# Performance work log

Measured on AMD Instinct MI355X. Metric: run time of the kernel, lower is better.

## Reference

```python
import jax, jax.numpy as jnp
import numpy as np

C = 768
H = 12
HD = C // H  # 64


def setup_inputs() -> dict:
    key = jax.random.key(0)
    k1, k2, k3, k4, k5, k6 = jax.random.split(key, 6)
    B, T = 8, 1024
    x = jax.random.normal(k1, (B, T, C), dtype=jnp.float32)
    mask = jax.random.randint(k2, (B, T), 0, 2, dtype=jnp.int32)
    # Linear params stored so that y = x @ W + b (W is [in, out])
    W_attn = jax.random.normal(k3, (C, 3 * C), dtype=jnp.float32) * 0.02
    b_attn = jax.random.normal(k4, (3 * C,), dtype=jnp.float32) * 0.02
    W_proj = jax.random.normal(k5, (C, C), dtype=jnp.float32) * 0.02
    b_proj = jax.random.normal(k6, (C,), dtype=jnp.float32) * 0.02
    return {"x": x, "mask": mask, "W_attn": W_attn, "b_attn": b_attn,
            "W_proj": W_proj, "b_proj": b_proj}


def reference(x, mask, W_attn, b_attn, W_proj, b_proj):
    B, T, _ = x.shape
    qkv = x @ W_attn + b_attn                      # [B, T, 3C]
    q, k, v = jnp.split(qkv, 3, axis=2)            # each [B, T, C]
    # [B, T, C] -> [B, H, T, HD]
    q = q.reshape(B, T, H, HD).transpose(0, 2, 1, 3)
    k = k.reshape(B, T, H, HD).transpose(0, 2, 1, 3)
    v = v.reshape(B, T, H, HD).transpose(0, 2, 1, 3)

    scale = 1.0 / np.sqrt(HD).astype(np.float32)
    att = jnp.einsum('bhqd,bhkd->bhqk', q, k) * scale  # [B, H, T, T]

    causal = jnp.tril(jnp.ones((T, T), dtype=bool))    # [T, T]
    att = jnp.where(causal[None, None], att, -jnp.inf)

    # custom mask: per-(batch, query-row) flag; where mask==0 the whole row
    # of scores is overwritten with 0.0001 (AFTER causal fill, as in torch)
    row_masked = (mask == 0)[:, None, :, None]         # [B, 1, T, 1]
    att = jnp.where(row_masked, jnp.float32(1e-4), att)

    att = jax.nn.softmax(att, axis=-1)
    # dropout layers are identity in eval mode
    y = jnp.einsum('bhqk,bhkd->bhqd', att, v)          # [B, H, T, HD]
    y = y.transpose(0, 2, 1, 3).reshape(B, T, C)
    y = y @ W_proj + b_proj
    return y
```

## Files before the change

kernel.cpp:

```cpp
#include <hip/hip_runtime.h>
#include <hip/hip_bf16.h>

#define BQ 8
#define TT 1024
#define CC 768
#define NH 12
#define HD 64
#define BH (BQ*NH)
#define MROWS (BQ*TT)
#define NQKV (3*CC)
#define KD CC

typedef unsigned short u16;
typedef __attribute__((ext_vector_type(4))) short short4v;
typedef __attribute__((ext_vector_type(8))) short short8v;
typedef __attribute__((ext_vector_type(4))) float floatx4;
typedef __attribute__((address_space(1))) const unsigned int gu32;
typedef __attribute__((address_space(3))) unsigned int lu32;

__device__ __forceinline__ float bf2f(u16 u) {
  union { unsigned int i; float f; } c; c.i = ((unsigned int)u) << 16; return c.f;
}
__device__ __forceinline__ u16 f2bf(float f) {
  union { __hip_bfloat16 h; u16 u; } c;
  c.h = __float2bfloat16(f);
  return c.u;
}
__device__ __forceinline__ float fast_exp2(float x) {
  return __builtin_amdgcn_exp2f(x);
}
__device__ __forceinline__ void async_ld16(const u16* g, u16* l) {
  __builtin_amdgcn_global_load_lds((gu32*)g, (lu32*)l, 16, 0, 0);
}

#define PREP_CONV 6144
#define PREP_WA   1728
#define PREP_WP   576
#define PREP_TOTAL (PREP_CONV + PREP_WA + PREP_WP)

__global__ __launch_bounds__(256) void prep_kernel(
    const float* __restrict__ x, u16* __restrict__ xb,
    const float* __restrict__ Wattn, u16* __restrict__ WtA,
    const float* __restrict__ Wproj, u16* __restrict__ WtP,
    float* __restrict__ mvz)
{
  __shared__ float tile[32][33];
  int bid = blockIdx.x;
  int tid = threadIdx.x;
  if (bid == PREP_TOTAL) {
    for (int i = tid; i < BH * HD; i += 256) mvz[i] = 0.f;
    return;
  }
  if (bid < PREP_CONV) {
    int i = (bid * 256 + tid) * 4;
    floatx4 v = *(const floatx4*)(x + i);
    short4v o;
    o[0] = (short)f2bf(v[0]); o[1] = (short)f2bf(v[1]);
    o[2] = (short)f2bf(v[2]); o[3] = (short)f2bf(v[3]);
    *(short4v*)(xb + i) = o;
    return;
  }
  const float* in; u16* out; int R, Cc, b2;
  if (bid < PREP_CONV + PREP_WA) { in = Wattn; out = WtA; R = KD; Cc = NQKV; b2 = bid - PREP_CONV; }
  else                           { in = Wproj; out = WtP; R = CC; Cc = CC;   b2 = bid - PREP_CONV - PREP_WA; }
  int ct = Cc >> 5;
  int bx = b2 % ct;
  int by = b2 / ct;
  int tx = tid & 31;
  int ty = tid >> 5;
  int c0 = bx << 5, r0 = by << 5;
#pragma unroll
  for (int s = 0; s < 4; ++s)
    tile[ty + s*8][tx] = in[(size_t)(r0 + ty + s*8) * Cc + c0 + tx];
  __syncthreads();
#pragma unroll
  for (int s = 0; s < 4; ++s)
    out[(size_t)(c0 + ty + s*8) * R + r0 + tx] = f2bf(tile[tx][ty + s*8]);
}

__global__ __launch_bounds__(256) void gemm_bt(
    const u16* __restrict__ A, const u16* __restrict__ Bt,
    const float* __restrict__ bias,
    float* __restrict__ out,
    u16* __restrict__ qo, u16* __restrict__ ko, u16* __restrict__ vo,
    float* __restrict__ mvp,
    int M, int N, int mode)
{
  __shared__ u16 smem[64 * 64 + 128 * 64];
  u16* Asm = smem;
  u16* Bsm = smem + 64 * 64;

  int tid = threadIdx.x;
  int lane = tid & 63;
  int w = tid >> 6;
  int c = lane & 15;
  int q4 = lane >> 4;

  int mtiles = M >> 6;
  int mt = blockIdx.x % mtiles;
  int nt = blockIdx.x / mtiles;
  int m0 = mt << 6, n0 = nt << 7;

  int wr = (w >> 1) << 5;
  int wc = (w & 1) << 6;

  int srow8 = lane >> 3;
  int ug = ((lane & 7) ^ srow8) << 3;
  const u16* ag = A  + (size_t)(m0 + w * 16 + srow8) * KD + ug;
  const u16* bg = Bt + (size_t)(n0 + w * 32 + srow8) * KD + ug;
  u16* asl = &Asm[(w * 16) * 64];
  u16* bsl = &Bsm[(w * 32) * 64];

  floatx4 acc[2][4];
#pragma unroll
  for (int mi = 0; mi < 2; ++mi)
#pragma unroll
    for (int ni = 0; ni < 4; ++ni) acc[mi][ni] = (floatx4){0.f, 0.f, 0.f, 0.f};

  int c7 = c & 7;

#pragma unroll 1
  for (int kt = 0; kt < KD; kt += 64) {
    async_ld16(ag + kt,              asl);
    async_ld16(ag + kt + 8 * KD,     asl + 8 * 64);
    async_ld16(bg + kt,              bsl);
    async_ld16(bg + kt + 8 * KD,     bsl + 8 * 64);
    async_ld16(bg + kt + 16 * KD,    bsl + 16 * 64);
    async_ld16(bg + kt + 24 * KD,    bsl + 24 * 64);
    __syncthreads();

    short8v af[2][2], bf[4][2];
#pragma unroll
    for (int kc = 0; kc < 2; ++kc) {
      int uoff = ((kc * 4 + q4) ^ c7) << 3;
#pragma unroll
      for (int mi = 0; mi < 2; ++mi)
        af[mi][kc] = *(const short8v*)&Asm[(wr + mi * 16 + c) * 64 + uoff];
#pragma unroll
      for (int ni = 0; ni < 4; ++ni)
        bf[ni][kc] = *(const short8v*)&Bsm[(wc + ni * 16 + c) * 64 + uoff];
    }
#pragma unroll
    for (int kc = 0; kc < 2; ++kc)
#pragma unroll
      for (int mi = 0; mi < 2; ++mi)
#pragma unroll
        for (int ni = 0; ni < 4; ++ni)
          acc[mi][ni] = __builtin_amdgcn_mfma_f32_16x16x32_bf16(af[mi][kc], bf[ni][kc], acc[mi][ni], 0, 0, 0);
    __syncthreads();
  }

  if (mode == 0) {
    int which = (n0 + wc) / CC;
    int nbase = (n0 + wc) - which * CC;
    int bb = m0 >> 10;
    int t0 = m0 & 1023;

    if (which < 2) {
      u16* dst0 = (which == 0) ? qo : ko;
#pragma unroll
      for (int ni = 0; ni < 4; ++ni) {
        int nn = nbase + ni * 16 + c;
        int hh = nn >> 6, dd = nn & 63;
        float bv = bias[which * CC + nn];
#pragma unroll
        for (int mi = 0; mi < 2; ++mi) {
#pragma unroll
          for (int r = 0; r < 4; ++r) {
            int tt2 = t0 + wr + mi * 16 + q4 * 4 + r;
            dst0[(((size_t)(bb * NH + hh)) * TT + tt2) * HD + dd] = f2bf(acc[mi][ni][r] + bv);
          }
        }
      }
    }
    if (n0 + 127 >= 2 * CC) {
      u16* Ct = smem;
      if (which == 2) {
#pragma unroll
        for (int ni = 0; ni < 4; ++ni) {
          float bv = bias[2 * CC + nbase + ni * 16 + c];
#pragma unroll
          for (int mi = 0; mi < 2; ++mi) {
            short4v pk;
#pragma unroll
            for (int r = 0; r < 4; ++r) pk[r] = (short)f2bf(acc[mi][ni][r] + bv);
            *(short4v*)&Ct[(wc + ni * 16 + c) * 72 + wr + mi * 16 + q4 * 4] = pk;
          }
        }
      }
      __syncthreads();
#pragma unroll
      for (int j = 0; j < 4; ++j) {
        int flat = tid + j * 256;
        int drow = flat >> 3, u = flat & 7;
        int nn2 = n0 + drow;
        if (nn2 >= 2 * CC) {
          int nv = nn2 - 2 * CC;
          int h2 = nv >> 6, d2 = nv & 63;
          short8v val = *(const short8v*)&Ct[drow * 72 + u * 8];
          *(short8v*)&vo[(((size_t)(bb * NH + h2)) * HD + d2) * TT + t0 + u * 8] = val;
        }
      }
      if (which == 2) {
        int hw = nbase >> 6;
        int bhw = bb * NH + hw;
#pragma unroll
        for (int ni = 0; ni < 4; ++ni) {
          float bv = bias[2 * CC + nbase + ni * 16 + c];
          float s = 8.0f * bv;
#pragma unroll
          for (int mi = 0; mi < 2; ++mi)
#pragma unroll
            for (int r = 0; r < 4; ++r) s += acc[mi][ni][r];
          s += __shfl_xor(s, 16);
          s += __shfl_xor(s, 32);
          if (q4 == 0) atomicAdd(&mvp[bhw * HD + ni * 16 + c], s);
        }
      }
    }
  } else {
#pragma unroll
    for (int ni = 0; ni < 4; ++ni) {
      int nn = n0 + wc + ni * 16 + c;
      float bv = bias[nn];
#pragma unroll
      for (int mi = 0; mi < 2; ++mi) {
#pragma unroll
        for (int r = 0; r < 4; ++r) {
          int mm = m0 + wr + mi * 16 + q4 * 4 + r;
          out[(size_t)mm * N + nn] = acc[mi][ni][r] + bv;
        }
      }
    }
  }
}

__global__ __launch_bounds__(256) void gemm_proj(
    const u16* __restrict__ A, const u16* __restrict__ Bt,
    const float* __restrict__ bias, float* __restrict__ out)
{
  __shared__ u16 As[64 * 64];
  __shared__ u16 Bs[64 * 64];

  int tid = threadIdx.x;
  int lane = tid & 63;
  int w = tid >> 6;
  int c = lane & 15;
  int q4 = lane >> 4;

  int mt = blockIdx.x & 127;
  int nt = blockIdx.x >> 7;
  int m0 = mt << 6, n0 = nt << 6;

  int wr = (w >> 1) << 5;
  int wc = (w & 1) << 5;

  int srow8 = lane >> 3;
  int ug = ((lane & 7) ^ srow8) << 3;
  const u16* ag = A  + (size_t)(m0 + w * 16 + srow8) * KD + ug;
  const u16* bg = Bt + (size_t)(n0 + w * 16 + srow8) * KD + ug;
  u16* asl = &As[(w * 16) * 64];
  u16* bsl = &Bs[(w * 16) * 64];

  floatx4 acc[2][2];
#pragma unroll
  for (int mi = 0; mi < 2; ++mi)
#pragma unroll
    for (int ni = 0; ni < 2; ++ni) acc[mi][ni] = (floatx4){0.f, 0.f, 0.f, 0.f};

  int c7 = c & 7;

#pragma unroll 1
  for (int kt = 0; kt < KD; kt += 64) {
    async_ld16(ag + kt,          asl);
    async_ld16(ag + kt + 8 * KD, asl + 8 * 64);
    async_ld16(bg + kt,          bsl);
    async_ld16(bg + kt + 8 * KD, bsl + 8 * 64);
    __syncthreads();

    short8v af[2][2], bf[2][2];
#pragma unroll
    for (int kc = 0; kc < 2; ++kc) {
      int uoff = ((kc * 4 + q4) ^ c7) << 3;
#pragma unroll
      for (int mi = 0; mi < 2; ++mi)
        af[mi][kc] = *(const short8v*)&As[(wr + mi * 16 + c) * 64 + uoff];
#pragma unroll
      for (int ni = 0; ni < 2; ++ni)
        bf[ni][kc] = *(const short8v*)&Bs[(wc + ni * 16 + c) * 64 + uoff];
    }
#pragma unroll
    for (int kc = 0; kc < 2; ++kc)
#pragma unroll
      for (int mi = 0; mi < 2; ++mi)
#pragma unroll
        for (int ni = 0; ni < 2; ++ni)
          acc[mi][ni] = __builtin_amdgcn_mfma_f32_16x16x32_bf16(af[mi][kc], bf[ni][kc], acc[mi][ni], 0, 0, 0);
    __syncthreads();
  }

#pragma unroll
  for (int ni = 0; ni < 2; ++ni) {
    int nn = n0 + wc + ni * 16 + c;
    float bv = bias[nn];
#pragma unroll
    for (int mi = 0; mi < 2; ++mi) {
#pragma unroll
      for (int r = 0; r < 4; ++r) {
        int mm = m0 + wr + mi * 16 + q4 * 4 + r;
        out[(size_t)mm * CC + nn] = acc[mi][ni][r] + bv;
      }
    }
  }
}

#define LDW 72
#define SCL 0.18033688f

__global__ __launch_bounds__(256, 3) void attn_kernel(
    const u16* __restrict__ qb, const u16* __restrict__ kb,
    const u16* __restrict__ vtb, const int* __restrict__ mask,
    const float* __restrict__ meanv,
    u16* __restrict__ outb)
{
  __shared__ u16 Ks[2][64 * LDW];
  __shared__ u16 Vs[2][64 * LDW];
  __shared__ u16 Ps[4][16 * LDW];

  int tid = threadIdx.x;
  int lane = tid & 63;
  int w = tid >> 6;
  int c = lane & 15;
  int q4 = lane >> 4;

  int lbid = ((blockIdx.x & 7) * 96) + (blockIdx.x >> 3);
  int pair = lbid & 7;
  int bh = lbid >> 3;
  int b = bh / NH;
  int h = bh - b * NH;

  int qtA = pair;
  int qtB = 15 - pair;
  int rowbaseA = (qtA << 6) + (w << 4);
  int rowbaseB = (qtB << 6) + (w << 4);

  int srow = tid >> 2;
  int schunk = (tid & 3) << 4;
  const u16* kgp = kb + ((size_t)bh * TT + srow) * HD + schunk;
  const u16* vgp = vtb + ((size_t)bh * HD + srow) * TT + schunk;
  u16* pw = &Ps[w][0];

  short8v onesv;
#pragma unroll
  for (int j = 0; j < 8; ++j) onesv[j] = (short)0x3F80;

  short8v qfA[2], qfB[2];
  {
    const u16* qpA = qb + ((size_t)bh * TT + rowbaseA + c) * HD + q4 * 8;
    qfA[0] = *(const short8v*)qpA;
    qfA[1] = *(const short8v*)(qpA + 32);
    const u16* qpB = qb + ((size_t)bh * TT + rowbaseB + c) * HD + q4 * 8;
    qfB[0] = *(const short8v*)qpB;
    qfB[1] = *(const short8v*)(qpB + 32);
  }

  floatx4 oA[4], oB[4];
#pragma unroll
  for (int i = 0; i < 4; ++i) {
    oA[i] = (floatx4){0.f, 0.f, 0.f, 0.f};
    oB[i] = (floatx4){0.f, 0.f, 0.f, 0.f};
  }
  floatx4 o5A = (floatx4){0.f, 0.f, 0.f, 0.f};
  floatx4 o5B = (floatx4){0.f, 0.f, 0.f, 0.f};

  short8v kr0 = *(const short8v*)kgp;
  short8v kr1 = *(const short8v*)(kgp + 8);
  short8v vr0 = *(const short8v*)vgp;
  short8v vr1 = *(const short8v*)(vgp + 8);
  {
    u16* kd = &Ks[0][srow * LDW + schunk];
    u16* vd = &Vs[0][srow * LDW + schunk];
    *(short8v*)kd = kr0; *(short8v*)(kd + 8) = kr1;
    *(short8v*)vd = vr0; *(short8v*)(vd + 8) = vr1;
  }

  int qrl = (w << 4) + c;

#pragma unroll 1
  for (int kt = 0; kt <= qtB; ++kt) {
    int cur = kt & 1;
    __syncthreads();

    if (kt < qtB) {
      const u16* kp = kgp + ((size_t)(kt + 1) << 6) * HD;
      const u16* vp = vgp + ((kt + 1) << 6);
      kr0 = *(const short8v*)kp;
      kr1 = *(const short8v*)(kp + 8);
      vr0 = *(const short8v*)vp;
      vr1 = *(const short8v*)(vp + 8);
    }

    bool doA = (kt <= qtA);

    floatx4 sA[4], sB[4];
#pragma unroll
    for (int nt = 0; nt < 4; ++nt) {
      sA[nt] = (floatx4){0.f, 0.f, 0.f, 0.f};
      sB[nt] = (floatx4){0.f, 0.f, 0.f, 0.f};
    }
    __builtin_amdgcn_s_setprio(1);
#pragma unroll
    for (int kc = 0; kc < 2; ++kc) {
#pragma unroll
      for (int nt = 0; nt < 4; ++nt) {
        short8v kf = *(const short8v*)&Ks[cur][(nt * 16 + c) * LDW + kc * 32 + q4 * 8];
        if (doA) sA[nt] = __builtin_amdgcn_mfma_f32_16x16x32_bf16(kf, qfA[kc], sA[nt], 0, 0, 0);
        sB[nt] = __builtin_amdgcn_mfma_f32_16x16x32_bf16(kf, qfB[kc], sB[nt], 0, 0, 0);
      }
    }
    __builtin_amdgcn_s_setprio(0);

    if (doA) {
#pragma unroll
      for (int nt = 0; nt < 4; ++nt) {
        short4v pk;
#pragma unroll
        for (int r = 0; r < 4; ++r) {
          float sv = sA[nt][r];
          if (kt == qtA && (nt * 16 + (q4 << 2) + r > qrl)) sv = -INFINITY;
          pk[r] = (short)f2bf(fast_exp2(sv * SCL));
        }
        *(short4v*)&pw[c * LDW + nt * 16 + (q4 << 2)] = pk;
      }
      __builtin_amdgcn_s_setprio(1);
#pragma unroll
      for (int kc = 0; kc < 2; ++kc) {
        short8v pf = *(const short8v*)&pw[c * LDW + kc * 32 + q4 * 8];
#pragma unroll
        for (int nt = 0; nt < 4; ++nt) {
          short8v vf = *(const short8v*)&Vs[cur][(nt * 16 + c) * LDW + kc * 32 + q4 * 8];
          oA[nt] = __builtin_amdgcn_mfma_f32_16x16x32_bf16(pf, vf, oA[nt], 0, 0, 0);
        }
        o5A = __builtin_amdgcn_mfma_f32_16x16x32_bf16(pf, onesv, o5A, 0, 0, 0);
      }
      __builtin_amdgcn_s_setprio(0);
    }

#pragma unroll
    for (int nt = 0; nt < 4; ++nt) {
      short4v pk;
#pragma unroll
      for (int r = 0; r < 4; ++r) {
        float sv = sB[nt][r];
        if (kt == qtB && (nt * 16 + (q4 << 2) + r > qrl)) sv = -INFINITY;
        pk[r] = (short)f2bf(fast_exp2(sv * SCL));
      }
      *(short4v*)&pw[c * LDW + nt * 16 + (q4 << 2)] = pk;
    }

    if (kt < qtB) {
      u16* kd = &Ks[cur ^ 1][srow * LDW + schunk];
      u16* vd = &Vs[cur ^ 1][srow * LDW + schunk];
      *(short8v*)kd = kr0; *(short8v*)(kd + 8) = kr1;
      *(short8v*)vd = vr0; *(short8v*)(vd + 8) = vr1;
    }

    __builtin_amdgcn_s_setprio(1);
#pragma unroll
    for (int kc = 0; kc < 2; ++kc) {
      short8v pf = *(const short8v*)&pw[c * LDW + kc * 32 + q4 * 8];
#pragma unroll
      for (int nt = 0; nt < 4; ++nt) {
        short8v vf = *(const short8v*)&Vs[cur][(nt * 16 + c) * LDW + kc * 32 + q4 * 8];
        oB[nt] = __builtin_amdgcn_mfma_f32_16x16x32_bf16(pf, vf, oB[nt], 0, 0, 0);
      }
      o5B = __builtin_amdgcn_mfma_f32_16x16x32_bf16(pf, onesv, o5B, 0, 0, 0);
    }
    __builtin_amdgcn_s_setprio(0);
  }

#pragma unroll
  for (int t = 0; t < 2; ++t) {
    int rowbase = t ? rowbaseB : rowbaseA;
    floatx4* o = t ? oB : oA;
    floatx4 o5 = t ? o5B : o5A;
    int qrow[4]; bool msk[4]; float inv[4];
#pragma unroll
    for (int r = 0; r < 4; ++r) {
      qrow[r] = rowbase + q4 * 4 + r;
      msk[r] = (mask[b * TT + qrow[r]] == 0);
      inv[r] = 1.f / o5[r];
    }
#pragma unroll
    for (int nt = 0; nt < 4; ++nt) {
      int d = nt * 16 + c;
      float mv = meanv[bh * HD + d] * 0.0009765625f;
#pragma unroll
      for (int r = 0; r < 4; ++r) {
        float val = msk[r] ? mv : o[nt][r] * inv[r];
        outb[((size_t)(b * TT + qrow[r])) * CC + h * HD + d] = f2bf(val);
      }
    }
  }
}

extern "C" void kernel_launch(void* const* d_in, const int* in_sizes, int n_in,
                              void* d_out, int out_size, void* d_ws, size_t ws_size,
                              hipStream_t stream)
{
  (void)in_sizes; (void)n_in; (void)out_size; (void)ws_size;
  const float* x     = (const float*)d_in[0];
  const int*   mask  = (const int*)d_in[1];
  const float* Wattn = (const float*)d_in[2];
  const float* battn = (const float*)d_in[3];
  const float* Wproj = (const float*)d_in[4];
  const float* bproj = (const float*)d_in[5];
  float* out = (float*)d_out;

  char* ws = (char*)d_ws;
  size_t off = 0;
  auto alloc = [&](size_t bytes) -> void* {
    void* p = ws + off;
    off += (bytes + 255) & ~(size_t)255;
    return p;
  };
  u16* WtA  = (u16*)alloc((size_t)NQKV * KD * 2);
  u16* WtP  = (u16*)alloc((size_t)CC * CC * 2);
  u16* xb   = (u16*)alloc((size_t)MROWS * CC * 2);
  u16* qbuf = (u16*)alloc((size_t)MROWS * CC * 2);
  u16* kbuf = (u16*)alloc((size_t)MROWS * CC * 2);
  u16* vtb  = (u16*)alloc((size_t)MROWS * CC * 2);
  u16* abuf = (u16*)alloc((size_t)MROWS * CC * 2);
  float* mv = (float*)alloc((size_t)BH * HD * 4);

  prep_kernel<<<PREP_TOTAL + 1, 256, 0, stream>>>(x, xb, Wattn, WtA, Wproj, WtP, mv);

  gemm_bt<<<(MROWS/64)*(NQKV/128), 256, 0, stream>>>(
      xb, WtA, battn, nullptr, qbuf, kbuf, vtb, mv, MROWS, NQKV, 0);

  attn_kernel<<<BH * 8, 256, 0, stream>>>(qbuf, kbuf, vtb, mask, mv, abuf);

  gemm_proj<<<(MROWS/64)*(CC/64), 256, 0, stream>>>(abuf, WtP, bproj, out);
}
```

Measured before the change: 179.1 us.

## Load K and V fragments directly from global memory, dropping LDS staging

Removes the double-buffered shared-memory staging of K and V tiles and the per-iteration block barrier. Each wave now reads its K and V MFMA operand fragments straight from global memory (relying on L1/L2 cache), with the V fragments held in registers for both the A and B passes. This trades LDS traffic and synchronisation for four-fold redundant global loads across waves, higher register pressure, and exposed load latency, since there is no explicit prefetch.

```diff
diff --git a/kernel.cpp b/kernel.cpp
--- a/kernel.cpp
+++ b/kernel.cpp
@@ -323,8 +323,6 @@
     const float* __restrict__ meanv,
     u16* __restrict__ outb)
 {
-  __shared__ u16 Ks[2][64 * LDW];
-  __shared__ u16 Vs[2][64 * LDW];
   __shared__ u16 Ps[4][16 * LDW];
 
   int tid = threadIdx.x;
@@ -344,10 +342,8 @@
   int rowbaseA = (qtA << 6) + (w << 4);
   int rowbaseB = (qtB << 6) + (w << 4);
 
-  int srow = tid >> 2;
-  int schunk = (tid & 3) << 4;
-  const u16* kgp = kb + ((size_t)bh * TT + srow) * HD + schunk;
-  const u16* vgp = vtb + ((size_t)bh * HD + srow) * TT + schunk;
+  const u16* kbase = kb + (size_t)bh * TT * HD;
+  const u16* vbase = vtb + (size_t)bh * HD * TT;
   u16* pw = &Ps[w][0];
 
   short8v onesv;
@@ -373,34 +369,19 @@
   floatx4 o5A = (floatx4){0.f, 0.f, 0.f, 0.f};
   floatx4 o5B = (floatx4){0.f, 0.f, 0.f, 0.f};
 
-  short8v kr0 = *(const short8v*)kgp;
-  short8v kr1 = *(const short8v*)(kgp + 8);
-  short8v vr0 = *(const short8v*)vgp;
-  short8v vr1 = *(const short8v*)(vgp + 8);
-  {
-    u16* kd = &Ks[0][srow * LDW + schunk];
-    u16* vd = &Vs[0][srow * LDW + schunk];
-    *(short8v*)kd = kr0; *(short8v*)(kd + 8) = kr1;
-    *(short8v*)vd = vr0; *(short8v*)(vd + 8) = vr1;
-  }
-
   int qrl = (w << 4) + c;
 
 #pragma unroll 1
   for (int kt = 0; kt <= qtB; ++kt) {
-    int cur = kt & 1;
-    __syncthreads();
-
-    if (kt < qtB) {
-      const u16* kp = kgp + ((size_t)(kt + 1) << 6) * HD;
-      const u16* vp = vgp + ((kt + 1) << 6);
-      kr0 = *(const short8v*)kp;
-      kr1 = *(const short8v*)(kp + 8);
-      vr0 = *(const short8v*)vp;
-      vr1 = *(const short8v*)(vp + 8);
-    }
-
     bool doA = (kt <= qtA);
+    int k0 = kt << 6;
+
+    short8v vfr[2][4];
+#pragma unroll
+    for (int kc = 0; kc < 2; ++kc)
+#pragma unroll
+      for (int nt = 0; nt < 4; ++nt)
+        vfr[kc][nt] = *(const short8v*)&vbase[(size_t)(nt * 16 + c) * TT + k0 + kc * 32 + q4 * 8];
 
     floatx4 sA[4], sB[4];
 #pragma unroll
@@ -413,7 +394,7 @@
     for (int kc = 0; kc < 2; ++kc) {
 #pragma unroll
       for (int nt = 0; nt < 4; ++nt) {
-        short8v kf = *(const short8v*)&Ks[cur][(nt * 16 + c) * LDW + kc * 32 + q4 * 8];
+        short8v kf = *(const short8v*)&kbase[(size_t)(k0 + nt * 16 + c) * HD + kc * 32 + q4 * 8];
         if (doA) sA[nt] = __builtin_amdgcn_mfma_f32_16x16x32_bf16(kf, qfA[kc], sA[nt], 0, 0, 0);
         sB[nt] = __builtin_amdgcn_mfma_f32_16x16x32_bf16(kf, qfB[kc], sB[nt], 0, 0, 0);
       }
@@ -437,10 +418,8 @@
       for (int kc = 0; kc < 2; ++kc) {
         short8v pf = *(const short8v*)&pw[c * LDW + kc * 32 + q4 * 8];
 #pragma unroll
-        for (int nt = 0; nt < 4; ++nt) {
-          short8v vf = *(const short8v*)&Vs[cur][(nt * 16 + c) * LDW + kc * 32 + q4 * 8];
-          oA[nt] = __builtin_amdgcn_mfma_f32_16x16x32_bf16(pf, vf, oA[nt], 0, 0, 0);
-        }
+        for (int nt = 0; nt < 4; ++nt)
+          oA[nt] = __builtin_amdgcn_mfma_f32_16x16x32_bf16(pf, vfr[kc][nt], oA[nt], 0, 0, 0);
         o5A = __builtin_amdgcn_mfma_f32_16x16x32_bf16(pf, onesv, o5A, 0, 0, 0);
       }
       __builtin_amdgcn_s_setprio(0);
@@ -458,22 +437,13 @@
       *(short4v*)&pw[c * LDW + nt * 16 + (q4 << 2)] = pk;
     }
 
-    if (kt < qtB) {
-      u16* kd = &Ks[cur ^ 1][srow * LDW + schunk];
-      u16* vd = &Vs[cur ^ 1][srow * LDW + schunk];
-      *(short8v*)kd = kr0; *(short8v*)(kd + 8) = kr1;
-      *(short8v*)vd = vr0; *(short8v*)(vd + 8) = vr1;
-    }
-
     __builtin_amdgcn_s_setprio(1);
 #pragma unroll
     for (int kc = 0; kc < 2; ++kc) {
       short8v pf = *(const short8v*)&pw[c * LDW + kc * 32 + q4 * 8];
 #pragma unroll
-      for (int nt = 0; nt < 4; ++nt) {
-        short8v vf = *(const short8v*)&Vs[cur][(nt * 16 + c) * LDW + kc * 32 + q4 * 8];
-        oB[nt] = __builtin_amdgcn_mfma_f32_16x16x32_bf16(pf, vf, oB[nt], 0, 0, 0);
-      }
+      for (int nt = 0; nt < 4; ++nt)
+        oB[nt] = __builtin_amdgcn_mfma_f32_16x16x32_bf16(pf, vfr[kc][nt], oB[nt], 0, 0, 0);
       o5B = __builtin_amdgcn_mfma_f32_16x16x32_bf16(pf, onesv, o5B, 0, 0, 0);
     }
     __builtin_amdgcn_s_setprio(0);
```

Measured after the change: 236.2 us. 1.32x slower.

## Pre-pack weights in MFMA fragment order and load B directly to registers

Applied to the files above, without the earlier changes.

The weight-prep kernel now writes the transposed bf16 weights in a packed layout that matches the MFMA B-fragment order (16-column by 32-k blocks). Both GEMM kernels then load B fragments straight from global memory into registers with one 16-byte load per lane, skipping the LDS staging and LDS reads for B. This cuts LDS traffic and footprint, which may help occupancy. The cost is that B loads are now synchronous global loads with no cross-wave reuse inside the block, so they depend on cache hits.

```diff
diff --git a/kernel.cpp b/kernel.cpp
--- a/kernel.cpp
+++ b/kernel.cpp
@@ -10,6 +10,7 @@
 #define MROWS (BQ*TT)
 #define NQKV (3*CC)
 #define KD CC
+#define KB5 (KD >> 5)
 
 typedef unsigned short u16;
 typedef __attribute__((ext_vector_type(4))) short short4v;
@@ -60,9 +61,9 @@
     *(short4v*)(xb + i) = o;
     return;
   }
-  const float* in; u16* out; int R, Cc, b2;
-  if (bid < PREP_CONV + PREP_WA) { in = Wattn; out = WtA; R = KD; Cc = NQKV; b2 = bid - PREP_CONV; }
-  else                           { in = Wproj; out = WtP; R = CC; Cc = CC;   b2 = bid - PREP_CONV - PREP_WA; }
+  const float* in; u16* out; int Cc, b2;
+  if (bid < PREP_CONV + PREP_WA) { in = Wattn; out = WtA; Cc = NQKV; b2 = bid - PREP_CONV; }
+  else                           { in = Wproj; out = WtP; Cc = CC;   b2 = bid - PREP_CONV - PREP_WA; }
   int ct = Cc >> 5;
   int bx = b2 % ct;
   int by = b2 / ct;
@@ -73,22 +74,27 @@
   for (int s = 0; s < 4; ++s)
     tile[ty + s*8][tx] = in[(size_t)(r0 + ty + s*8) * Cc + c0 + tx];
   __syncthreads();
-#pragma unroll
-  for (int s = 0; s < 4; ++s)
-    out[(size_t)(c0 + ty + s*8) * R + r0 + tx] = f2bf(tile[tx][ty + s*8]);
+  if (tid < 128) {
+    int n_loc = tid & 31, kq = tid >> 5;
+    int n = c0 + n_loc;
+    short8v o8;
+#pragma unroll
+    for (int j = 0; j < 8; ++j) o8[j] = (short)f2bf(tile[kq * 8 + j][n_loc]);
+    size_t dst = ((size_t)(n >> 4) * KB5 + (r0 >> 5)) * 512 + kq * 128 + (n & 15) * 8;
+    *(short8v*)&out[dst] = o8;
+  }
 }
 
 __global__ __launch_bounds__(256) void gemm_bt(
-    const u16* __restrict__ A, const u16* __restrict__ Bt,
+    const u16* __restrict__ A, const u16* __restrict__ BtF,
     const float* __restrict__ bias,
     float* __restrict__ out,
     u16* __restrict__ qo, u16* __restrict__ ko, u16* __restrict__ vo,
     float* __restrict__ mvp,
     int M, int N, int mode)
 {
-  __shared__ u16 smem[64 * 64 + 128 * 64];
+  __shared__ u16 smem[128 * 72];
   u16* Asm = smem;
-  u16* Bsm = smem + 64 * 64;
 
   int tid = threadIdx.x;
   int lane = tid & 63;
@@ -106,10 +112,10 @@
 
   int srow8 = lane >> 3;
   int ug = ((lane & 7) ^ srow8) << 3;
-  const u16* ag = A  + (size_t)(m0 + w * 16 + srow8) * KD + ug;
-  const u16* bg = Bt + (size_t)(n0 + w * 32 + srow8) * KD + ug;
+  const u16* ag = A + (size_t)(m0 + w * 16 + srow8) * KD + ug;
   u16* asl = &Asm[(w * 16) * 64];
-  u16* bsl = &Bsm[(w * 32) * 64];
+
+  const u16* bF = BtF + ((size_t)((n0 + wc) >> 4) * KB5) * 512 + (lane << 3);
 
   floatx4 acc[2][4];
 #pragma unroll
@@ -121,24 +127,25 @@
 
 #pragma unroll 1
   for (int kt = 0; kt < KD; kt += 64) {
-    async_ld16(ag + kt,              asl);
-    async_ld16(ag + kt + 8 * KD,     asl + 8 * 64);
-    async_ld16(bg + kt,              bsl);
-    async_ld16(bg + kt + 8 * KD,     bsl + 8 * 64);
-    async_ld16(bg + kt + 16 * KD,    bsl + 16 * 64);
-    async_ld16(bg + kt + 24 * KD,    bsl + 24 * 64);
+    async_ld16(ag + kt,          asl);
+    async_ld16(ag + kt + 8 * KD, asl + 8 * 64);
+
+    short8v bf[4][2];
+#pragma unroll
+    for (int kc = 0; kc < 2; ++kc)
+#pragma unroll
+      for (int ni = 0; ni < 4; ++ni)
+        bf[ni][kc] = *(const short8v*)(bF + ((size_t)(ni * KB5 + (kt >> 5) + kc) << 9));
+
     __syncthreads();
 
-    short8v af[2][2], bf[4][2];
+    short8v af[2][2];
 #pragma unroll
     for (int kc = 0; kc < 2; ++kc) {
       int uoff = ((kc * 4 + q4) ^ c7) << 3;
 #pragma unroll
       for (int mi = 0; mi < 2; ++mi)
         af[mi][kc] = *(const short8v*)&Asm[(wr + mi * 16 + c) * 64 + uoff];
-#pragma unroll
-      for (int ni = 0; ni < 4; ++ni)
-        bf[ni][kc] = *(const short8v*)&Bsm[(wc + ni * 16 + c) * 64 + uoff];
     }
 #pragma unroll
     for (int kc = 0; kc < 2; ++kc)
@@ -236,11 +243,10 @@
 }
 
 __global__ __launch_bounds__(256) void gemm_proj(
-    const u16* __restrict__ A, const u16* __restrict__ Bt,
+    const u16* __restrict__ A, const u16* __restrict__ BtF,
     const float* __restrict__ bias, float* __restrict__ out)
 {
   __shared__ u16 As[64 * 64];
-  __shared__ u16 Bs[64 * 64];
 
   int tid = threadIdx.x;
   int lane = tid & 63;
@@ -257,10 +263,10 @@
 
   int srow8 = lane >> 3;
   int ug = ((lane & 7) ^ srow8) << 3;
-  const u16* ag = A  + (size_t)(m0 + w * 16 + srow8) * KD + ug;
-  const u16* bg = Bt + (size_t)(n0 + w * 16 + srow8) * KD + ug;
+  const u16* ag = A + (size_t)(m0 + w * 16 + srow8) * KD + ug;
   u16* asl = &As[(w * 16) * 64];
-  u16* bsl = &Bs[(w * 16) * 64];
+
+  const u16* bF = BtF + ((size_t)((n0 + wc) >> 4) * KB5) * 512 + (lane << 3);
 
   floatx4 acc[2][2];
 #pragma unroll
@@ -274,20 +280,23 @@
   for (int kt = 0; kt < KD; kt += 64) {
     async_ld16(ag + kt,          asl);
     async_ld16(ag + kt + 8 * KD, asl + 8 * 64);
-    async_ld16(bg + kt,          bsl);
-    async_ld16(bg + kt + 8 * KD, bsl + 8 * 64);
+
+    short8v bf[2][2];
+#pragma unroll
+    for (int kc = 0; kc < 2; ++kc)
+#pragma unroll
+      for (int ni = 0; ni < 2; ++ni)
+        bf[ni][kc] = *(const short8v*)(bF + ((size_t)(ni * KB5 + (kt >> 5) + kc) << 9));
+
     __syncthreads();
 
-    short8v af[2][2], bf[2][2];
+    short8v af[2][2];
 #pragma unroll
     for (int kc = 0; kc < 2; ++kc) {
       int uoff = ((kc * 4 + q4) ^ c7) << 3;
 #pragma unroll
       for (int mi = 0; mi < 2; ++mi)
         af[mi][kc] = *(const short8v*)&As[(wr + mi * 16 + c) * 64 + uoff];
-#pragma unroll
-      for (int ni = 0; ni < 2; ++ni)
-        bf[ni][kc] = *(const short8v*)&Bs[(wc + ni * 16 + c) * 64 + uoff];
     }
 #pragma unroll
     for (int kc = 0; kc < 2; ++kc)
```

New measurement: 185.9 us. 1.04x slower.
